# Kernel tuning notes

Measured on AMD Instinct MI355X. Metric: run time of the kernel, lower is better.

Reference implementation:

```python
import jax, jax.numpy as jnp
import numpy as np

I, H, O, T = 512, 2048, 512, 4096

def setup_inputs() -> dict:
    key = jax.random.key(0)
    ks = jax.random.split(key, 7)
    s = 0.02  # small init scale to avoid gate saturation
    return {
        "input_seq": jax.random.normal(ks[0], (T, I), dtype=jnp.float32),
        "W_ih": jax.random.normal(ks[1], (4 * H, I), dtype=jnp.float32) * s,
        "W_hh": jax.random.normal(ks[2], (4 * H, H), dtype=jnp.float32) * s,
        "b_ih": jax.random.normal(ks[3], (4 * H,), dtype=jnp.float32) * s,
        "b_hh": jax.random.normal(ks[4], (4 * H,), dtype=jnp.float32) * s,
        "W_lin": jax.random.normal(ks[5], (O, H), dtype=jnp.float32) * s,
        "b_lin": jax.random.normal(ks[6], (O,), dtype=jnp.float32) * s,
    }

def reference(input_seq, W_ih, W_hh, b_ih, b_hh, W_lin, b_lin):
    # Single-layer LSTM, batch=1, initial (h, c) = 0; PyTorch gate order i,f,g,o.
    b = b_ih + b_hh
    # Precompute input projections for all timesteps: (T, 4H)
    xz = input_seq @ W_ih.T + b

    def step(carry, xz_t):
        h, c = carry
        z = xz_t + h @ W_hh.T  # (4H,)
        i, f, g, o = jnp.split(z, 4)
        i = jax.nn.sigmoid(i)
        f = jax.nn.sigmoid(f)
        g = jnp.tanh(g)
        o = jax.nn.sigmoid(o)
        c = f * c + i * g
        h = o * jnp.tanh(c)
        return (h, c), None

    h0 = jnp.zeros((H,), dtype=input_seq.dtype)
    c0 = jnp.zeros((H,), dtype=input_seq.dtype)
    (hT, _), _ = jax.lax.scan(step, (h0, c0), xz)
    # predictions[-1] == linear(lstm_out[-1]) == linear(h_T)
    return hT @ W_lin.T + b_lin
```

## Files before the change

kernel.cpp:

```cpp
#include <hip/hip_runtime.h>


#define TSTEPS 4096
#define HDIM   2048
#define GDIM   8192
#define IDIM   512
#define ODIM   512

#define XZ_BYTES ((size_t)TSTEPS * GDIM * sizeof(float))

typedef int int4v __attribute__((ext_vector_type(4)));

__device__ __forceinline__ float sigmoidf_fast(float x) {
    return 1.0f / (1.0f + __expf(-x));
}
__device__ __forceinline__ float tanhf_fast(float x) {
    return 2.0f / (1.0f + __expf(-2.0f * x)) - 1.0f;
}

__device__ __forceinline__ void poll4(const int4v* p0, const int4v* p1,
                                      const int4v* p2, const int4v* p3,
                                      int4v& a, int4v& b, int4v& c, int4v& d)
{
    asm volatile(
        "global_load_dwordx4 %0, %4, off sc0 sc1\n\t"
        "global_load_dwordx4 %1, %5, off sc0 sc1\n\t"
        "global_load_dwordx4 %2, %6, off sc0 sc1\n\t"
        "global_load_dwordx4 %3, %7, off sc0 sc1\n\t"
        "s_waitcnt vmcnt(0)"
        : "=&v"(a), "=&v"(b), "=&v"(c), "=&v"(d)
        : "v"(p0), "v"(p1), "v"(p2), "v"(p3)
        : "memory");
}
__device__ __forceinline__ void store_line(int4v* p, int4v v)
{
    asm volatile("global_store_dwordx4 %0, %1, off sc0 sc1"
                 :: "v"(p), "v"(v) : "memory");
}

__global__ __launch_bounds__(256) void xz_gemm(
    const float* __restrict__ A, const float* __restrict__ B,
    const float* __restrict__ bih, const float* __restrict__ bhh,
    float* __restrict__ C)
{
    __shared__ float As[16][132];
    __shared__ float Bs[16][132];

    const int tid = threadIdx.x;
    const int m0 = blockIdx.y * 128;
    const int n0 = blockIdx.x * 128;
    const int tx = tid & 15;
    const int ty = tid >> 4;

    const int lrow  = tid >> 1;
    const int kbase = (tid & 1) * 8;

    float acc[8][8] = {};

    for (int k0 = 0; k0 < IDIM; k0 += 16) {
        const float4 av0 = *(const float4*)(A + (size_t)(m0 + lrow) * IDIM + k0 + kbase);
        const float4 av1 = *(const float4*)(A + (size_t)(m0 + lrow) * IDIM + k0 + kbase + 4);
        const float4 bv0 = *(const float4*)(B + (size_t)(n0 + lrow) * IDIM + k0 + kbase);
        const float4 bv1 = *(const float4*)(B + (size_t)(n0 + lrow) * IDIM + k0 + kbase + 4);

        __syncthreads();
        As[kbase + 0][lrow] = av0.x; As[kbase + 1][lrow] = av0.y;
        As[kbase + 2][lrow] = av0.z; As[kbase + 3][lrow] = av0.w;
        As[kbase + 4][lrow] = av1.x; As[kbase + 5][lrow] = av1.y;
        As[kbase + 6][lrow] = av1.z; As[kbase + 7][lrow] = av1.w;
        Bs[kbase + 0][lrow] = bv0.x; Bs[kbase + 1][lrow] = bv0.y;
        Bs[kbase + 2][lrow] = bv0.z; Bs[kbase + 3][lrow] = bv0.w;
        Bs[kbase + 4][lrow] = bv1.x; Bs[kbase + 5][lrow] = bv1.y;
        Bs[kbase + 6][lrow] = bv1.z; Bs[kbase + 7][lrow] = bv1.w;
        __syncthreads();

#pragma unroll
        for (int kk = 0; kk < 16; ++kk) {
            const float4 a0 = *(const float4*)&As[kk][ty * 8];
            const float4 a1 = *(const float4*)&As[kk][ty * 8 + 4];
            const float4 b0 = *(const float4*)&Bs[kk][tx * 8];
            const float4 b1 = *(const float4*)&Bs[kk][tx * 8 + 4];
            const float ar[8] = {a0.x, a0.y, a0.z, a0.w, a1.x, a1.y, a1.z, a1.w};
            const float br[8] = {b0.x, b0.y, b0.z, b0.w, b1.x, b1.y, b1.z, b1.w};
#pragma unroll
            for (int i = 0; i < 8; ++i)
#pragma unroll
                for (int jj = 0; jj < 8; ++jj)
                    acc[i][jj] = fmaf(ar[i], br[jj], acc[i][jj]);
        }
    }

    float bias[8];
#pragma unroll
    for (int jj = 0; jj < 8; ++jj) {
        const int n = n0 + tx * 8 + jj;
        bias[jj] = bih[n] + bhh[n];
    }
#pragma unroll
    for (int i = 0; i < 8; ++i) {
        float* crow = C + (size_t)(m0 + ty * 8 + i) * GDIM + n0 + tx * 8;
        float4 v0, v1;
        v0.x = acc[i][0] + bias[0]; v0.y = acc[i][1] + bias[1];
        v0.z = acc[i][2] + bias[2]; v0.w = acc[i][3] + bias[3];
        v1.x = acc[i][4] + bias[4]; v1.y = acc[i][5] + bias[5];
        v1.z = acc[i][6] + bias[6]; v1.w = acc[i][7] + bias[7];
        ((float4*)crow)[0] = v0;
        ((float4*)crow)[1] = v1;
    }
}

__global__ __launch_bounds__(256, 1) void lstm_rec(
    const float* __restrict__ Whh, const float* __restrict__ xz,
    int4v* __restrict__ lines)
{
    __shared__ float hsh[2 * 2080];

    const int tidb = threadIdx.x;
    const int tid  = blockIdx.x * 256 + tidb;
    const int j    = tid >> 5;
    const int g    = (tid >> 3) & 3;
    const int ck   = tid & 7;
    const int row  = g * HDIM + j;
    const int wv   = tidb >> 6;
    const int ln   = tidb & 63;

    const float4* wsrc = (const float4*)(Whh + (size_t)row * HDIM + ck * 256);
    float4 w[64];
#pragma unroll
    for (int i = 0; i < 64; ++i) w[i] = wsrc[i];

    const bool owner = (tid & 31) == 0;
    float cstate = 0.0f;

    int4v*       sl0 = lines + (blockIdx.x * 4 + wv);
    int4v*       sl1 = sl0 + 1024;
    const int4v* cb0 = lines + 256 * wv + ln;
    const int4v* cb1 = cb0 + 1024;

    float zx = xz[row];

    unsigned cap = 1u << 21;

    for (int t = 0; t < TSTEPS; ++t) {
        int4v v0, v1, v2, v3;
        {
            const unsigned need = (unsigned)t;
            const int4v* cb = (t & 1) ? cb1 : cb0;
            unsigned spins = 0;
            for (;;) {
                poll4(cb, cb + 64, cb + 128, cb + 192, v0, v1, v2, v3);
                const bool ok =
                    ((unsigned)v0.y >= need) & ((unsigned)v0.w >= need) &
                    ((unsigned)v1.y >= need) & ((unsigned)v1.w >= need) &
                    ((unsigned)v2.y >= need) & ((unsigned)v2.w >= need) &
                    ((unsigned)v3.y >= need) & ((unsigned)v3.w >= need);
                if (ok) break;
                __builtin_amdgcn_s_sleep(1);
                if (++spins > cap) { cap = 2048; break; }
            }
        }

        const int buf = t & 1;
        const int b0  = buf * 2080 + (2 * wv) * 260;
        const int b1  = b0 + 260;
        *(float2*)&hsh[b0 +       2 * ln] = make_float2(__int_as_float(v0.x), __int_as_float(v0.z));
        *(float2*)&hsh[b0 + 128 + 2 * ln] = make_float2(__int_as_float(v1.x), __int_as_float(v1.z));
        *(float2*)&hsh[b1 +       2 * ln] = make_float2(__int_as_float(v2.x), __int_as_float(v2.z));
        *(float2*)&hsh[b1 + 128 + 2 * ln] = make_float2(__int_as_float(v3.x), __int_as_float(v3.z));
        __syncthreads();

        const int tn = (t + 1 < TSTEPS) ? (t + 1) : (TSTEPS - 1);
        const float zx_next = xz[(size_t)tn * GDIM + row];

        const float4* hr = (const float4*)(hsh + buf * 2080 + ck * 260);
        float a0 = 0.f, a1 = 0.f, a2 = 0.f, a3 = 0.f;
#pragma unroll
        for (int i = 0; i < 64; ++i) {
            const float4 h4 = hr[i];
            a0 = fmaf(w[i].x, h4.x, a0);
            a1 = fmaf(w[i].y, h4.y, a1);
            a2 = fmaf(w[i].z, h4.z, a2);
            a3 = fmaf(w[i].w, h4.w, a3);
        }
        float d = (a0 + a1) + (a2 + a3);
        d += __shfl_xor(d, 1);
        d += __shfl_xor(d, 2);
        d += __shfl_xor(d, 4);
        const float z  = d + zx;
        const float zf = __shfl_xor(z, 8);
        const float zg = __shfl_xor(z, 16);
        const float zo = __shfl_xor(z, 24);

        float hval = 0.0f;
        if (owner) {
            const float ig = sigmoidf_fast(z);
            const float fg = sigmoidf_fast(zf);
            const float gg = tanhf_fast(zg);
            const float og = sigmoidf_fast(zo);
            cstate = fmaf(fg, cstate, ig * gg);
            hval = og * tanhf_fast(cstate);
        }
        const float h1 = __shfl(hval, 32);
        if (ln == 0) {
            int4v sv;
            sv.x = __float_as_int(hval); sv.y = t + 1;
            sv.z = __float_as_int(h1);   sv.w = t + 1;
            store_line(((t + 1) & 1) ? sl1 : sl0, sv);
        }
        zx = zx_next;
    }
}

__global__ __launch_bounds__(256) void final_linear(
    const float* __restrict__ Wlin, const float* __restrict__ blin,
    const int4v* __restrict__ hl, float* __restrict__ out)
{
    const int wid  = (blockIdx.x * 256 + threadIdx.x) >> 6;
    const int lane = threadIdx.x & 63;
    const float4* wr = (const float4*)(Wlin + (size_t)wid * HDIM);
    float acc = 0.f;
#pragma unroll
    for (int i = 0; i < 8; ++i) {
        const int k = lane + 64 * i;
        const float4 w4 = wr[k];
        const int4v la = hl[2 * k];
        const int4v lb = hl[2 * k + 1];
        acc += w4.x * __int_as_float(la.x) + w4.y * __int_as_float(la.z)
             + w4.z * __int_as_float(lb.x) + w4.w * __int_as_float(lb.z);
    }
#pragma unroll
    for (int off = 32; off > 0; off >>= 1) acc += __shfl_down(acc, off);
    if (lane == 0) out[wid] = acc + blin[wid];
}

extern "C" void kernel_launch(void* const* d_in, const int* in_sizes, int n_in,
                              void* d_out, int out_size, void* d_ws, size_t ws_size,
                              hipStream_t stream) {
    const float* input = (const float*)d_in[0];
    const float* Wih   = (const float*)d_in[1];
    const float* Whh   = (const float*)d_in[2];
    const float* bih   = (const float*)d_in[3];
    const float* bhh   = (const float*)d_in[4];
    const float* Wlin  = (const float*)d_in[5];
    const float* blin  = (const float*)d_in[6];
    float* out = (float*)d_out;

    char* ws = (char*)d_ws;
    float* xz    = (float*)ws;
    int4v* lines = (int4v*)(ws + XZ_BYTES);

    hipMemsetAsync(lines, 0, 2 * 1024 * sizeof(int4v), stream);

    dim3 ggrid(GDIM / 128, TSTEPS / 128);
    xz_gemm<<<ggrid, 256, 0, stream>>>(input, Wih, bih, bhh, xz);

    lstm_rec<<<dim3(256), dim3(256), 0, stream>>>(Whh, xz, lines);

    final_linear<<<ODIM / 4, 256, 0, stream>>>(Wlin, blin, lines, out);
}
```

Baseline: 16.37 ms.

## Relay per-XCD hidden-state broadcast through an L2-local mirror

One block per XCD is elected through an atomic claim counter to act as relay. The relay polls the global h lines at system coherence (sc0 sc1) and copies them into an XCD-local mirror using L2-scope stores. The other blocks on that XCD then poll the mirror with L2-scope loads instead of going to memory. The aim is to cut cross-XCD polling traffic and latency in the per-timestep barrier, at the cost of an extra relay hop. It also relies on blocks of one XCD sharing an L2, with a timeout fallback to direct polling.

```diff
diff --git a/kernel.cpp b/kernel.cpp
--- a/kernel.cpp
+++ b/kernel.cpp
@@ -18,9 +18,9 @@
     return 2.0f / (1.0f + __expf(-2.0f * x)) - 1.0f;
 }
 
-__device__ __forceinline__ void poll4(const int4v* p0, const int4v* p1,
-                                      const int4v* p2, const int4v* p3,
-                                      int4v& a, int4v& b, int4v& c, int4v& d)
+__device__ __forceinline__ void poll4_mall(const int4v* p0, const int4v* p1,
+                                           const int4v* p2, const int4v* p3,
+                                           int4v& a, int4v& b, int4v& c, int4v& d)
 {
     asm volatile(
         "global_load_dwordx4 %0, %4, off sc0 sc1\n\t"
@@ -32,10 +32,39 @@
         : "v"(p0), "v"(p1), "v"(p2), "v"(p3)
         : "memory");
 }
+__device__ __forceinline__ void poll4_l2(const int4v* p0, const int4v* p1,
+                                         const int4v* p2, const int4v* p3,
+                                         int4v& a, int4v& b, int4v& c, int4v& d)
+{
+    asm volatile(
+        "global_load_dwordx4 %0, %4, off sc0\n\t"
+        "global_load_dwordx4 %1, %5, off sc0\n\t"
+        "global_load_dwordx4 %2, %6, off sc0\n\t"
+        "global_load_dwordx4 %3, %7, off sc0\n\t"
+        "s_waitcnt vmcnt(0)"
+        : "=&v"(a), "=&v"(b), "=&v"(c), "=&v"(d)
+        : "v"(p0), "v"(p1), "v"(p2), "v"(p3)
+        : "memory");
+}
 __device__ __forceinline__ void store_line(int4v* p, int4v v)
 {
     asm volatile("global_store_dwordx4 %0, %1, off sc0 sc1"
                  :: "v"(p), "v"(v) : "memory");
+}
+__device__ __forceinline__ void store_line_l2(int4v* p, int4v v)
+{
+    asm volatile("global_store_dwordx4 %0, %1, off sc0"
+                 :: "v"(p), "v"(v) : "memory");
+}
+
+__device__ __forceinline__ bool tags_ok(const int4v& v0, const int4v& v1,
+                                        const int4v& v2, const int4v& v3,
+                                        unsigned need)
+{
+    return ((unsigned)v0.y >= need) & ((unsigned)v0.w >= need) &
+           ((unsigned)v1.y >= need) & ((unsigned)v1.w >= need) &
+           ((unsigned)v2.y >= need) & ((unsigned)v2.w >= need) &
+           ((unsigned)v3.y >= need) & ((unsigned)v3.w >= need);
 }
 
 __global__ __launch_bounds__(256) void xz_gemm(
@@ -111,9 +140,11 @@
 
 __global__ __launch_bounds__(256, 1) void lstm_rec(
     const float* __restrict__ Whh, const float* __restrict__ xz,
-    int4v* __restrict__ lines)
+    int4v* __restrict__ lines, int4v* __restrict__ mirror,
+    unsigned* __restrict__ claim)
 {
     __shared__ float hsh[2 * 2080];
+    __shared__ unsigned relayflag;
 
     const int tidb = threadIdx.x;
     const int tid  = blockIdx.x * 256 + tidb;
@@ -124,10 +155,23 @@
     const int wv   = tidb >> 6;
     const int ln   = tidb & 63;
 
+    unsigned myxcd;
+    asm volatile("s_getreg_b32 %0, hwreg(HW_REG_XCC_ID)" : "=s"(myxcd));
+    myxcd &= 7;
+
+    if (tidb == 0) {
+        const unsigned r = __hip_atomic_fetch_add(&claim[myxcd], 1u,
+                               __ATOMIC_RELAXED, __HIP_MEMORY_SCOPE_AGENT);
+        relayflag = (r == 0) ? 1u : 0u;
+    }
+
     const float4* wsrc = (const float4*)(Whh + (size_t)row * HDIM + ck * 256);
     float4 w[64];
 #pragma unroll
     for (int i = 0; i < 64; ++i) w[i] = wsrc[i];
+
+    __syncthreads();
+    const bool isRelay = (relayflag != 0);
 
     const bool owner = (tid & 31) == 0;
     float cstate = 0.0f;
@@ -136,27 +180,48 @@
     int4v*       sl1 = sl0 + 1024;
     const int4v* cb0 = lines + 256 * wv + ln;
     const int4v* cb1 = cb0 + 1024;
+    int4v* mibase = mirror + ((size_t)myxcd << 11) + 256 * wv + ln;
 
     float zx = xz[row];
 
-    unsigned cap = 1u << 21;
+    unsigned capg  = 1u << 21;
+    bool     direct = false;
 
     for (int t = 0; t < TSTEPS; ++t) {
         int4v v0, v1, v2, v3;
         {
             const unsigned need = (unsigned)t;
-            const int4v* cb = (t & 1) ? cb1 : cb0;
-            unsigned spins = 0;
-            for (;;) {
-                poll4(cb, cb + 64, cb + 128, cb + 192, v0, v1, v2, v3);
-                const bool ok =
-                    ((unsigned)v0.y >= need) & ((unsigned)v0.w >= need) &
-                    ((unsigned)v1.y >= need) & ((unsigned)v1.w >= need) &
-                    ((unsigned)v2.y >= need) & ((unsigned)v2.w >= need) &
-                    ((unsigned)v3.y >= need) & ((unsigned)v3.w >= need);
-                if (ok) break;
-                __builtin_amdgcn_s_sleep(1);
-                if (++spins > cap) { cap = 2048; break; }
+            const int par = t & 1;
+            const int4v* gb = par ? cb1 : cb0;
+            if (isRelay) {
+                unsigned spins = 0;
+                for (;;) {
+                    poll4_mall(gb, gb + 64, gb + 128, gb + 192, v0, v1, v2, v3);
+                    if (tags_ok(v0, v1, v2, v3, need)) break;
+                    __builtin_amdgcn_s_sleep(1);
+                    if (++spins > capg) { capg = 2048; break; }
+                }
+                int4v* mb = mibase + ((size_t)par << 10);
+                store_line_l2(mb,       v0);
+                store_line_l2(mb + 64,  v1);
+                store_line_l2(mb + 128, v2);
+                store_line_l2(mb + 192, v3);
+            } else {
+                const int4v* mb = mibase + ((size_t)par << 10);
+                unsigned spins = 0;
+                for (;;) {
+                    if (!direct) {
+                        poll4_l2(mb, mb + 64, mb + 128, mb + 192, v0, v1, v2, v3);
+                        if (tags_ok(v0, v1, v2, v3, need)) break;
+                        __builtin_amdgcn_s_sleep(1);
+                        if (++spins > 4096) { direct = true; spins = 0; }
+                    } else {
+                        poll4_mall(gb, gb + 64, gb + 128, gb + 192, v0, v1, v2, v3);
+                        if (tags_ok(v0, v1, v2, v3, need)) break;
+                        __builtin_amdgcn_s_sleep(1);
+                        if (++spins > capg) { capg = 2048; break; }
+                    }
+                }
             }
         }
 
@@ -246,15 +311,17 @@
     float* out = (float*)d_out;
 
     char* ws = (char*)d_ws;
-    float* xz    = (float*)ws;
-    int4v* lines = (int4v*)(ws + XZ_BYTES);
-
-    hipMemsetAsync(lines, 0, 2 * 1024 * sizeof(int4v), stream);
+    float* xz      = (float*)ws;
+    int4v* lines   = (int4v*)(ws + XZ_BYTES);
+    int4v* mirror  = (int4v*)(ws + XZ_BYTES + 32768);
+    unsigned* claim = (unsigned*)(ws + XZ_BYTES + 32768 + 262144);
+
+    hipMemsetAsync(lines, 0, 32768 + 262144 + 64, stream);
 
     dim3 ggrid(GDIM / 128, TSTEPS / 128);
     xz_gemm<<<ggrid, 256, 0, stream>>>(input, Wih, bih, bhh, xz);
 
-    lstm_rec<<<dim3(256), dim3(256), 0, stream>>>(Whh, xz, lines);
+    lstm_rec<<<dim3(256), dim3(256), 0, stream>>>(Whh, xz, lines, mirror, claim);
 
     final_linear<<<ODIM / 4, 256, 0, stream>>>(Wlin, blin, lines, out);
 }
```

New measurement: 17.66 ms. +7.8%, slower.
